# Kernel optimization log

Measured on AMD Instinct MI355X. Metric: run time of the kernel, lower is better.

The kernel has to match this reference:

```python
import jax, jax.numpy as jnp
import numpy as np
import math

N_CELLS = 16384
INPUT_DIM = 512
HIDDEN = 512


def build_neighbors(n):
    n_bits = max(1, int(math.ceil(math.log2(n))))
    idx = np.arange(n)
    flips = [idx ^ (1 << b) for b in range(n_bits)]
    ring = [(idx + 1) % n, (idx - 1) % n]
    allnb = np.stack(flips + ring, axis=1)
    # dedupe per row; for power-of-2 n every row has exactly n_bits+1 uniques
    rows = [sorted(set(r.tolist())) for r in allnb]
    return np.asarray(rows, dtype=np.int32)


def setup_inputs() -> dict:
    key = jax.random.key(0)
    ks = jax.random.split(key, 12)
    n, d, h = N_CELLS, INPUT_DIM, HIDDEN
    amp = jax.random.uniform(ks[0], (n, h)) * 0.5 + 0.5
    phase = jax.random.normal(ks[1], (n, h)) * 0.3 + (2 * math.pi * jnp.arange(n) / n)[:, None]
    return {
        "x": jax.random.normal(ks[2], (1, d), dtype=jnp.float32),
        "pump_W": jax.random.normal(ks[3], (n, d), dtype=jnp.float32) / np.sqrt(d),
        "pump_b": jax.random.normal(ks[4], (n,), dtype=jnp.float32) * 0.01,
        "dec_W": jax.random.normal(ks[5], (d, 2 * h), dtype=jnp.float32) / np.sqrt(2 * h),
        "dec_b": jax.random.normal(ks[6], (d,), dtype=jnp.float32) * 0.01,
        "cs_re": (amp * jnp.cos(phase)).astype(jnp.float32),
        "cs_im": (amp * jnp.sin(phase)).astype(jnp.float32),
        "excited": jax.random.uniform(ks[7], (n,)) * 0.6,  # some cells above 0.5 threshold
        "phase_vel": jax.random.normal(ks[8], (n, h), dtype=jnp.float32) * 0.05,
        "cav_re": jax.random.normal(ks[9], (h,), dtype=jnp.float32) * 0.01,
        "cav_im": jax.random.normal(ks[10], (h,), dtype=jnp.float32) * 0.01,
        "neighbors": jnp.asarray(build_neighbors(n)),
    }


def reference(x, pump_W, pump_b, dec_W, dec_b, cs_re, cs_im, excited, phase_vel, cav_re, cav_im, neighbors):
    states = (cs_re + 1j * cs_im).astype(jnp.complex64)          # [n,h]
    cavity = (cav_re + 1j * cav_im).astype(jnp.complex64)        # [h]

    # pump + excited fraction update
    pump = jax.nn.sigmoid(x @ pump_W.T + pump_b)[0]              # [n]
    excited = jnp.clip(excited * 0.95 + pump * 0.05, 0.0, 1.0)

    # free phase rotation: polar(1, 0.1*phase_vel)
    states = states * jnp.exp(1j * (phase_vel * 0.1)).astype(jnp.complex64)

    # neighbor phase coupling (hypercube + ring, k=15 neighbors each)
    ang = jnp.angle(states)                                      # [n,h]
    nb_states = states[neighbors]                                # [n,k,h]
    coupling = jnp.cos(ang[:, None, :] - ang[neighbors])         # [n,k,h]
    interference = 0.1 * jnp.sum(coupling * nb_states, axis=1)   # [n,h]
    k = neighbors.shape[1]
    new_states = 0.7 * states + 0.3 * interference / k

    # lasing: population inversion threshold
    lasing = excited > 0.5                                       # [n]
    n_lasing = jnp.sum(lasing)
    maskf = lasing.astype(jnp.float32)[:, None]
    # emission uses pre-phase-lock states (torch copies lasing_cells first)
    emission = jnp.sum(new_states * maskf, axis=0) / jnp.maximum(n_lasing, 1).astype(jnp.float32)
    cavity_new = jnp.where(n_lasing > 0, 0.8 * cavity + 0.2 * emission, cavity)

    # phase-lock lasing cells to (old) cavity phase
    cavity_phase = jnp.angle(cavity)                             # old cavity
    new_ang = jnp.angle(new_states)
    locked = 0.3 * cavity_phase[None, :] + 0.7 * new_ang
    locked_states = jnp.abs(new_states) * jnp.exp(1j * locked)
    new_states = jnp.where(lasing[:, None], locked_states.astype(jnp.complex64), new_states)
    excited = jnp.where(lasing, excited * 0.9, excited * 0.98)

    # cavity feedback (updated cavity) + amplitude renorm
    new_states = new_states + 0.05 * cavity_new[None, :]
    amp = jnp.abs(new_states)
    amp = amp / (jnp.max(amp, axis=-1, keepdims=True) + 1e-8)
    final_states = (amp * jnp.exp(1j * jnp.angle(new_states))).astype(jnp.complex64)

    # decode cavity mode
    out_real = jnp.concatenate([cavity_new.real, cavity_new.imag])[None, :].astype(jnp.float32)  # [1,2h]
    pred = out_real @ dec_W.T + dec_b                            # [1, input_dim]
    tension = jnp.var(jnp.abs(final_states))
    return pred, tension
```

## Files before the change

kernel.cpp:

```cpp
#include <hip/hip_runtime.h>
#include <hip/hip_fp16.h>
#include <math.h>

#define N_CELLS 16384
#define HID 512
#define IND 512

#define ROT_BLOCKS  2048
#define PUMP_BLOCKS 1024

#define CPB 16
#define CELL_BLOCKS (N_CELLS / CPB)
#define PRED_BLOCKS 128

#define CNT_OFF   0
#define LASB_OFF  1024
#define EMIS_OFF  8192
#define CAV_OFF   16384
#define VPART_OFF 32768
#define ROT_OFF   (1<<20)
#define NST_OFF   (ROT_OFF + (size_t)N_CELLS*HID*4)

typedef unsigned int u32;

__device__ inline __half2 u2h(u32 u) { union { u32 u; __half2 h; } x; x.u = u; return x.h; }
__device__ inline u32 h2u(__half2 h) { union { u32 u; __half2 h; } x; x.h = h; return x.u; }
__device__ inline u32 packh2(float re, float im) { return h2u(__floats2half2_rn(re, im)); }
__device__ inline float2 unph2(u32 u) { __half2 h = u2h(u); return make_float2(__low2float(h), __high2float(h)); }

#if __has_builtin(__builtin_amdgcn_fdot2)
typedef _Float16 hv2 __attribute__((ext_vector_type(2)));
__device__ inline float dot2u(u32 a, u32 b) {
    union { u32 u; hv2 h; } x, y; x.u = a; y.u = b;
    return __builtin_amdgcn_fdot2(x.h, y.h, 0.f, false);
}
#else
__device__ inline float dot2u(u32 a, u32 b) {
    float2 af = unph2(a), bf = unph2(b);
    return fmaf(af.x, bf.x, af.y * bf.y);
}
#endif

__device__ inline void accnb(__half2& acc, u32 y, u32 q) {
    float d = dot2u(y, q);
    acc = __hfma2(__float2half2_rn(d), u2h(q), acc);
}

__device__ inline u32 fincell(u32 y, __half2 acc, int las, float& emR, float& emI) {
    float2 yf = unph2(y);
    float a  = fmaf(yf.x, yf.x, yf.y * yf.y);
    float rs = rsqrtf(a);
    float sq = a * rs;
    float2 af = make_float2(__low2float(acc), __high2float(acc));
    float nr = 0.7f * sq * yf.x + 0.002f * rs * af.x;
    float ni = 0.7f * sq * yf.y + 0.002f * rs * af.y;
    if (las) { emR += nr; emI += ni; }
    return packh2(nr, ni);
}

__device__ inline u32 rot1(float re, float im, float w) {
    float sc = rsqrtf(sqrtf(fmaf(re, re, im * im)));
    float s, c;
    __sincosf(0.1f * w, &s, &c);
    return packh2((re * c - im * s) * sc, (re * s + im * c) * sc);
}

__device__ inline float dot4(float4 a, float4 b) {
    return a.x * b.x + a.y * b.y + a.z * b.z + a.w * b.w;
}

__global__ __launch_bounds__(256, 3) void k_front(const float* __restrict__ cr,
        const float* __restrict__ ci, const float* __restrict__ pv,
        u32* __restrict__ yt,
        const float* __restrict__ x, const float* __restrict__ pW,
        const float* __restrict__ pb, const float* __restrict__ excited,
        u32* __restrict__ lasb) {
    int b = blockIdx.x, tid = threadIdx.x;
    if (b < ROT_BLOCKS) {
        __shared__ u32 tile[64 * 65];
        int cb = b >> 3, hb = b & 7;
        const float4* cr4 = (const float4*)cr;
        const float4* ci4 = (const float4*)ci;
        const float4* pv4 = (const float4*)pv;
        float4 A[4], Bv[4], Wv[4];
        int row[4], c4[4];
#pragma unroll
        for (int j = 0; j < 4; ++j) {
            int idx = tid + 256 * j;
            row[j] = idx >> 4; c4[j] = idx & 15;
            size_t g = (size_t)(cb * 64 + row[j]) * 128 + hb * 16 + c4[j];
            A[j] = cr4[g]; Bv[j] = ci4[g]; Wv[j] = pv4[g];
        }
        __builtin_amdgcn_sched_barrier(0);
#pragma unroll
        for (int j = 0; j < 4; ++j) {
            u32* dst = &tile[row[j] * 65 + (c4[j] << 2)];
            dst[0] = rot1(A[j].x, Bv[j].x, Wv[j].x);
            dst[1] = rot1(A[j].y, Bv[j].y, Wv[j].y);
            dst[2] = rot1(A[j].z, Bv[j].z, Wv[j].z);
            dst[3] = rot1(A[j].w, Bv[j].w, Wv[j].w);
        }
        __syncthreads();
        uint4 v[4];
#pragma unroll
        for (int j = 0; j < 4; ++j) {
            int idx = tid + 256 * j;
            int chr = idx >> 4, q = idx & 15;
            v[j].x = tile[(q * 4 + 0) * 65 + chr];
            v[j].y = tile[(q * 4 + 1) * 65 + chr];
            v[j].z = tile[(q * 4 + 2) * 65 + chr];
            v[j].w = tile[(q * 4 + 3) * 65 + chr];
        }
#pragma unroll
        for (int j = 0; j < 4; ++j) {
            int idx = tid + 256 * j;
            int chr = idx >> 4, q = idx & 15;
            ((uint4*)(yt + (size_t)(hb * 64 + chr) * N_CELLS + cb * 64))[q] = v[j];
        }
    } else {
        int c0 = (b - ROT_BLOCKS) * 16;
        int cell = c0 + (tid >> 4);
        int l16 = tid & 15;
        int lane = tid & 63;
        const float4* w4 = (const float4*)(pW + (size_t)cell * IND);
        const float4* x4 = (const float4*)x;
        float4 wv[8];
#pragma unroll
        for (int k = 0; k < 8; ++k) wv[k] = w4[l16 + 16 * k];
        __builtin_amdgcn_sched_barrier(0);
        float acc = 0.f;
#pragma unroll
        for (int k = 0; k < 8; ++k) acc += dot4(wv[k], x4[l16 + 16 * k]);
#pragma unroll
        for (int o = 1; o < 16; o <<= 1) acc += __shfl_xor(acc, o, 64);
        int flag = 0;
        if (l16 == 0) {
            float p = 1.f / (1.f + expf(-(acc + pb[cell])));
            float e = excited[cell] * 0.95f + p * 0.05f;
            e = fminf(fmaxf(e, 0.f), 1.f);
            flag = (e > 0.5f) ? 1 : 0;
        }
        unsigned long long bal = __ballot(flag);
        if (lane == 0) {
            u32 val = (u32)(bal & 1) | ((u32)(bal >> 16) & 1) << 1
                    | ((u32)(bal >> 32) & 1) << 2 | ((u32)(bal >> 48) & 1) << 3;
            atomicOr(&lasb[cell >> 5], val << (cell & 31));
        }
    }
}

__global__ __launch_bounds__(1024, 8) void k_coup(const u32* __restrict__ yt,
                                                  const u32* __restrict__ lasb,
                                                  u32* __restrict__ nstT,
                                                  float2* __restrict__ emisT,
                                                  const float* __restrict__ cavr,
                                                  const float* __restrict__ cavi,
                                                  float* __restrict__ cavws,
                                                  int* __restrict__ cnt) {
    __shared__ __align__(16) u32 col[N_CELLS];
    int ch = blockIdx.x, tid = threadIdx.x;
    const uint4* src = (const uint4*)(yt + (size_t)ch * N_CELLS);
    uint4* cdst = (uint4*)col;
    {
        uint4 st[4];
#pragma unroll
        for (int k = 0; k < 4; ++k) st[k] = src[tid + 1024 * k];
        __builtin_amdgcn_sched_barrier(0);
#pragma unroll
        for (int k = 0; k < 4; ++k) cdst[tid + 1024 * k] = st[k];
    }
    __syncthreads();

    float emR = 0.f, emI = 0.f;
    int nlo = 0;
    uint4* outp = (uint4*)(nstT + (size_t)ch * N_CELLS);
#pragma unroll 2
    for (int j = 0; j < 4; ++j) {
        int s = tid + 1024 * j;
        u32 f = (lasb[s >> 3] >> ((s & 7) * 4)) & 0xF;
        int c = s << 2;
        uint4 sq = *(const uint4*)&col[c];
        __half2 z = __floats2half2_rn(0.f, 0.f);
        __half2 a0 = z, a1 = z, a2 = z, a3 = z;
#pragma unroll
        for (int bb = 2; bb < 14; ++bb) {
            uint4 q = *(const uint4*)&col[c ^ (1 << bb)];
            accnb(a0, sq.x, q.x);
            accnb(a1, sq.y, q.y);
            accnb(a2, sq.z, q.z);
            accnb(a3, sq.w, q.w);
        }
        u32 qm = col[(c - 1) & (N_CELLS - 1)];
        u32 qp = col[(c + 4) & (N_CELLS - 1)];
        accnb(a0, sq.x, sq.y); accnb(a0, sq.x, sq.z); accnb(a0, sq.x, qm);
        accnb(a1, sq.y, sq.x); accnb(a1, sq.y, sq.w); accnb(a1, sq.y, sq.z);
        accnb(a2, sq.z, sq.w); accnb(a2, sq.z, sq.x); accnb(a2, sq.z, sq.y);
        accnb(a3, sq.w, sq.z); accnb(a3, sq.w, sq.y); accnb(a3, sq.w, qp);
        nlo += __popc(f);
        uint4 ov;
        ov.x = fincell(sq.x, a0, f & 1, emR, emI);
        ov.y = fincell(sq.y, a1, f & 2, emR, emI);
        ov.z = fincell(sq.z, a2, f & 4, emR, emI);
        ov.w = fincell(sq.w, a3, f & 8, emR, emI);
        outp[s] = ov;
    }
    __syncthreads();
#pragma unroll
    for (int o = 32; o; o >>= 1) {
        emR += __shfl_xor(emR, o, 64);
        emI += __shfl_xor(emI, o, 64);
        nlo += __shfl_xor(nlo, o, 64);
    }
    float* scr = (float*)col;
    int* iscr = (int*)col;
    int wid = tid >> 6, lane = tid & 63;
    if (lane == 0) { scr[wid] = emR; scr[16 + wid] = emI; iscr[32 + wid] = nlo; }
    __syncthreads();
    if (tid == 0) {
        float sr = 0.f, si = 0.f; int sn = 0;
#pragma unroll
        for (int k = 0; k < 16; ++k) { sr += scr[k]; si += scr[16 + k]; sn += iscr[32 + k]; }
        emisT[ch] = make_float2(sr, si);
        iscr[48] = sn;
        __threadfence();
        int old = atomicAdd(cnt, 1);
        iscr[49] = (old == HID - 1) ? 1 : 0;
    }
    __syncthreads();
    if (iscr[49]) {
        __threadfence();
        int nl = iscr[48];
        float inv = (nl > 0) ? 0.2f / (float)nl : 0.f;
        if (tid < 512) {
            int i = tid;
            float crv = cavr[i], civ = cavi[i];
            float2 e = emisT[i];
            cavws[i]        = (nl > 0) ? 0.8f * crv + e.x * inv : crv;
            cavws[512 + i]  = (nl > 0) ? 0.8f * civ + e.y * inv : civ;
            cavws[1024 + i] = atan2f(civ, crv);
        }
    }
}

__global__ __launch_bounds__(256, 2) void k_finall(const u32* __restrict__ nstT,
        const u32* __restrict__ lasb, const float* __restrict__ cavws,
        const float* __restrict__ dW, const float* __restrict__ db,
        float2* __restrict__ vpart, int* __restrict__ cnt2,
        float* __restrict__ out) {
    int b = blockIdx.x, t = threadIdx.x;
    int wid = t >> 6, lane = t & 63;
    if (b < CELL_BLOCKS) {
        __shared__ __align__(16) u32 tile[CPB * HID];
        __shared__ __align__(16) float scav[1536];
        __shared__ float w1[4], w2[4];
        __shared__ int slast;
        __shared__ double l1s[4], l2s[4];

        int c0 = b * CPB;
        uint4 ld[8]; int chv[8], qv[8];
#pragma unroll
        for (int j = 0; j < 8; ++j) {
            int idx = t + 256 * j;
            chv[j] = idx >> 2; qv[j] = idx & 3;
            ld[j] = ((const uint4*)(nstT + (size_t)chv[j] * N_CELLS + c0))[qv[j]];
        }
        const float4* c4p = (const float4*)cavws;
#pragma unroll
        for (int k2 = 0; k2 < 2; ++k2) {
            int i = t + 256 * k2;
            if (i < 384) ((float4*)scav)[i] = c4p[i];
        }
        __builtin_amdgcn_sched_barrier(0);
#pragma unroll
        for (int j = 0; j < 8; ++j) {
#pragma unroll
            for (int e = 0; e < 4; ++e) {
                int cell = qv[j] * 4 + e;
                int sw = chv[j] ^ (((e ^ qv[j]) & 1) << 4);
                tile[cell * HID + sw] = ((const u32*)&ld[j])[e];
            }
        }
        __syncthreads();

        int cell = t >> 4, kk = t & 15;
        int cg = c0 + cell;
        int lasc = (lasb[cg >> 5] >> (cg & 31)) & 1;
        int swb = ((cell ^ (cell >> 2)) & 1) << 4;
        const u32* trow = &tile[cell * HID];
        float sa = 0.f, sa2 = 0.f, mx = 0.f;
#pragma unroll 8
        for (int i = 0; i < 32; ++i) {
            int ch = kk + 16 * i;
            float2 vf = unph2(trow[ch ^ swb]);
            float vx = vf.x, vy = vf.y;
            if (lasc) {
                float r = sqrtf(fmaf(vx, vx, vy * vy));
                float lk = 0.3f * scav[1024 + ch] + 0.7f * atan2f(vy, vx);
                float sn, cs;
                __sincosf(lk, &sn, &cs);
                vx = r * cs; vy = r * sn;
            }
            vx += 0.05f * scav[ch];
            vy += 0.05f * scav[512 + ch];
            float a2v = fmaf(vx, vx, vy * vy);
            float a = sqrtf(a2v);
            sa += a; sa2 += a2v; mx = fmaxf(mx, a);
        }
#pragma unroll
        for (int o = 1; o < 16; o <<= 1) {
            sa += __shfl_xor(sa, o, 64);
            sa2 += __shfl_xor(sa2, o, 64);
            mx = fmaxf(mx, __shfl_xor(mx, o, 64));
        }
        float invm = 1.f / (mx + 1e-8f);
        float s1 = sa * invm, s2 = sa2 * invm * invm;
        s1 += __shfl_xor(s1, 16, 64); s2 += __shfl_xor(s2, 16, 64);
        s1 += __shfl_xor(s1, 32, 64); s2 += __shfl_xor(s2, 32, 64);
        if (lane == 0) { w1[wid] = s1; w2[wid] = s2; }
        __syncthreads();
        if (t == 0) {
            vpart[b] = make_float2(w1[0] + w1[1] + w1[2] + w1[3],
                                   w2[0] + w2[1] + w2[2] + w2[3]);
            __threadfence();
            int old = atomicAdd(cnt2, 1);
            slast = (old == CELL_BLOCKS - 1) ? 1 : 0;
        }
        __syncthreads();
        if (slast) {
            __threadfence();
            double d1 = (double)vpart[t].x + (double)vpart[t + 256].x
                      + (double)vpart[t + 512].x + (double)vpart[t + 768].x;
            double d2 = (double)vpart[t].y + (double)vpart[t + 256].y
                      + (double)vpart[t + 512].y + (double)vpart[t + 768].y;
#pragma unroll
            for (int o = 32; o; o >>= 1) { d1 += __shfl_xor(d1, o, 64); d2 += __shfl_xor(d2, o, 64); }
            if (lane == 0) { l1s[wid] = d1; l2s[wid] = d2; }
            __syncthreads();
            if (t == 0) {
                double t1 = l1s[0] + l1s[1] + l1s[2] + l1s[3];
                double t2 = l2s[0] + l2s[1] + l2s[2] + l2s[3];
                double nn = (double)N_CELLS * (double)HID;
                double mean = t1 / nn;
                out[IND] = (float)(t2 / nn - mean * mean);
            }
        }
    } else {
        int j = (b - CELL_BLOCKS) * 4 + wid;
        const float4* w4 = (const float4*)(dW + (size_t)j * (2 * HID));
        const float4* o4 = (const float4*)cavws;
        float a2 = 0.f;
#pragma unroll
        for (int tt = 0; tt < 4; ++tt) {
            float4 a = w4[lane + 64 * tt];
            float4 bx = o4[lane + 64 * tt];
            a2 += a.x * bx.x + a.y * bx.y + a.z * bx.z + a.w * bx.w;
        }
#pragma unroll
        for (int o = 32; o; o >>= 1) a2 += __shfl_xor(a2, o, 64);
        if (lane == 0) out[j] = a2 + db[j];
    }
}

extern "C" void kernel_launch(void* const* d_in, const int* in_sizes, int n_in,
                              void* d_out, int out_size, void* d_ws, size_t ws_size,
                              hipStream_t stream) {
    const float* x       = (const float*)d_in[0];
    const float* pump_W  = (const float*)d_in[1];
    const float* pump_b  = (const float*)d_in[2];
    const float* dec_W   = (const float*)d_in[3];
    const float* dec_b   = (const float*)d_in[4];
    const float* cs_re   = (const float*)d_in[5];
    const float* cs_im   = (const float*)d_in[6];
    const float* excited = (const float*)d_in[7];
    const float* pvel    = (const float*)d_in[8];
    const float* cav_re  = (const float*)d_in[9];
    const float* cav_im  = (const float*)d_in[10];

    float* out = (float*)d_out;
    char* ws = (char*)d_ws;
    int*    cnt   = (int*)(ws + CNT_OFF);
    u32*    lasb  = (u32*)(ws + LASB_OFF);
    float2* emisT = (float2*)(ws + EMIS_OFF);
    float*  cavws = (float*)(ws + CAV_OFF);
    float2* vpart = (float2*)(ws + VPART_OFF);
    u32*    yt    = (u32*)(ws + ROT_OFF);
    u32*    nstT  = (u32*)(ws + NST_OFF);

    hipMemsetAsync(ws, 0, 4096, stream);
    k_front<<<ROT_BLOCKS + PUMP_BLOCKS, 256, 0, stream>>>(
        cs_re, cs_im, pvel, yt, x, pump_W, pump_b, excited, lasb);
    k_coup<<<HID, 1024, 0, stream>>>(yt, lasb, nstT, emisT, cav_re, cav_im, cavws, cnt);
    k_finall<<<CELL_BLOCKS + PRED_BLOCKS, 256, 0, stream>>>(
        nstT, lasb, cavws, dec_W, dec_b, vpart, cnt + 1, out);
}
```

Before: 264.5 us.

## Stage global loads directly into LDS and retile rotation and final kernels

Replaces register-staged global-to-shared copies with direct global_load_lds transfers in the rotation, coupling and finalize kernels. The rotation stage is retiled into smaller 64x32 tiles with twice as many blocks. The finalize kernel now uses a channel-major tile layout, so the per-cell max and sum reductions go through shared memory. Launch bounds are raised for higher occupancy. The aim is to cut VGPR pressure and LDS transpose overhead, at the cost of more LDS use and reliance on the LDS-direct load builtin.

```diff
diff --git a/kernel.cpp b/kernel.cpp
--- a/kernel.cpp
+++ b/kernel.cpp
@@ -6,7 +6,7 @@
 #define HID 512
 #define IND 512
 
-#define ROT_BLOCKS  2048
+#define ROT_BLOCKS  4096
 #define PUMP_BLOCKS 1024
 
 #define CPB 16
@@ -40,6 +40,17 @@
     return fmaf(af.x, bf.x, af.y * bf.y);
 }
 #endif
+
+__device__ inline void cp16(const void* g, void* l) {
+#if __has_builtin(__builtin_amdgcn_global_load_lds)
+    char* base = (char*)l - (size_t)((threadIdx.x & 63) * 16);
+    __builtin_amdgcn_global_load_lds(
+        (const __attribute__((address_space(1))) unsigned int*)g,
+        (__attribute__((address_space(3))) unsigned int*)base, 16, 0, 0);
+#else
+    *(uint4*)l = *(const uint4*)g;
+#endif
+}
 
 __device__ inline void accnb(__half2& acc, u32 y, u32 q) {
     float d = dot2u(y, q);
@@ -69,7 +80,7 @@
     return a.x * b.x + a.y * b.y + a.z * b.z + a.w * b.w;
 }
 
-__global__ __launch_bounds__(256, 3) void k_front(const float* __restrict__ cr,
+__global__ __launch_bounds__(256, 4) void k_front(const float* __restrict__ cr,
         const float* __restrict__ ci, const float* __restrict__ pv,
         u32* __restrict__ yt,
         const float* __restrict__ x, const float* __restrict__ pW,
@@ -77,45 +88,50 @@
         u32* __restrict__ lasb) {
     int b = blockIdx.x, tid = threadIdx.x;
     if (b < ROT_BLOCKS) {
-        __shared__ u32 tile[64 * 65];
-        int cb = b >> 3, hb = b & 7;
-        const float4* cr4 = (const float4*)cr;
-        const float4* ci4 = (const float4*)ci;
-        const float4* pv4 = (const float4*)pv;
-        float4 A[4], Bv[4], Wv[4];
-        int row[4], c4[4];
-#pragma unroll
-        for (int j = 0; j < 4; ++j) {
-            int idx = tid + 256 * j;
-            row[j] = idx >> 4; c4[j] = idx & 15;
-            size_t g = (size_t)(cb * 64 + row[j]) * 128 + hb * 16 + c4[j];
-            A[j] = cr4[g]; Bv[j] = ci4[g]; Wv[j] = pv4[g];
-        }
-        __builtin_amdgcn_sched_barrier(0);
-#pragma unroll
-        for (int j = 0; j < 4; ++j) {
-            u32* dst = &tile[row[j] * 65 + (c4[j] << 2)];
-            dst[0] = rot1(A[j].x, Bv[j].x, Wv[j].x);
-            dst[1] = rot1(A[j].y, Bv[j].y, Wv[j].y);
-            dst[2] = rot1(A[j].z, Bv[j].z, Wv[j].z);
-            dst[3] = rot1(A[j].w, Bv[j].w, Wv[j].w);
-        }
-        __syncthreads();
-        uint4 v[4];
-#pragma unroll
-        for (int j = 0; j < 4; ++j) {
-            int idx = tid + 256 * j;
-            int chr = idx >> 4, q = idx & 15;
-            v[j].x = tile[(q * 4 + 0) * 65 + chr];
-            v[j].y = tile[(q * 4 + 1) * 65 + chr];
-            v[j].z = tile[(q * 4 + 2) * 65 + chr];
-            v[j].w = tile[(q * 4 + 3) * 65 + chr];
-        }
-#pragma unroll
-        for (int j = 0; j < 4; ++j) {
-            int idx = tid + 256 * j;
-            int chr = idx >> 4, q = idx & 15;
-            ((uint4*)(yt + (size_t)(hb * 64 + chr) * N_CELLS + cb * 64))[q] = v[j];
+        __shared__ __align__(16) float sA[2048], sB[2048], sW[2048];
+        __shared__ __align__(16) u32 tile[32 * 65];
+        int cb = b >> 4, hb = b & 15;
+        size_t goff = (size_t)cb * 64 * 2048 + (size_t)hb * 128;
+        const char* gA = (const char*)cr + goff;
+        const char* gB = (const char*)ci + goff;
+        const char* gW = (const char*)pv + goff;
+#pragma unroll
+        for (int k = 0; k < 2; ++k) {
+            int o = tid * 16 + k * 4096;
+            size_t go = (size_t)(o >> 7) * 2048 + (o & 127);
+            cp16(gA + go, (char*)sA + o);
+            cp16(gB + go, (char*)sB + o);
+            cp16(gW + go, (char*)sW + o);
+        }
+        __syncthreads();
+        int cell = tid >> 2, q = tid & 3;
+        const float4* a4 = (const float4*)sA + cell * 8 + q * 2;
+        const float4* b4 = (const float4*)sB + cell * 8 + q * 2;
+        const float4* w4 = (const float4*)sW + cell * 8 + q * 2;
+        float4 A0 = a4[0], A1 = a4[1];
+        float4 B0 = b4[0], B1 = b4[1];
+        float4 W0 = w4[0], W1 = w4[1];
+        int ch8 = q * 8;
+        u32* tp = &tile[cell];
+        tp[(ch8 + 0) * 65] = rot1(A0.x, B0.x, W0.x);
+        tp[(ch8 + 1) * 65] = rot1(A0.y, B0.y, W0.y);
+        tp[(ch8 + 2) * 65] = rot1(A0.z, B0.z, W0.z);
+        tp[(ch8 + 3) * 65] = rot1(A0.w, B0.w, W0.w);
+        tp[(ch8 + 4) * 65] = rot1(A1.x, B1.x, W1.x);
+        tp[(ch8 + 5) * 65] = rot1(A1.y, B1.y, W1.y);
+        tp[(ch8 + 6) * 65] = rot1(A1.z, B1.z, W1.z);
+        tp[(ch8 + 7) * 65] = rot1(A1.w, B1.w, W1.w);
+        __syncthreads();
+#pragma unroll
+        for (int g2 = 0; g2 < 2; ++g2) {
+            int idx = tid + 256 * g2;
+            int chr = idx >> 4, c4 = idx & 15;
+            uint4 v;
+            v.x = tile[chr * 65 + c4 * 4 + 0];
+            v.y = tile[chr * 65 + c4 * 4 + 1];
+            v.z = tile[chr * 65 + c4 * 4 + 2];
+            v.w = tile[chr * 65 + c4 * 4 + 3];
+            ((uint4*)(yt + (size_t)(hb * 32 + chr) * N_CELLS + cb * 64))[c4] = v;
         }
     } else {
         int c0 = (b - ROT_BLOCKS) * 16;
@@ -127,7 +143,6 @@
         float4 wv[8];
 #pragma unroll
         for (int k = 0; k < 8; ++k) wv[k] = w4[l16 + 16 * k];
-        __builtin_amdgcn_sched_barrier(0);
         float acc = 0.f;
 #pragma unroll
         for (int k = 0; k < 8; ++k) acc += dot4(wv[k], x4[l16 + 16 * k]);
@@ -159,16 +174,10 @@
                                                   int* __restrict__ cnt) {
     __shared__ __align__(16) u32 col[N_CELLS];
     int ch = blockIdx.x, tid = threadIdx.x;
-    const uint4* src = (const uint4*)(yt + (size_t)ch * N_CELLS);
-    uint4* cdst = (uint4*)col;
-    {
-        uint4 st[4];
-#pragma unroll
-        for (int k = 0; k < 4; ++k) st[k] = src[tid + 1024 * k];
-        __builtin_amdgcn_sched_barrier(0);
-#pragma unroll
-        for (int k = 0; k < 4; ++k) cdst[tid + 1024 * k] = st[k];
-    }
+    const char* gsrc = (const char*)(yt + (size_t)ch * N_CELLS);
+#pragma unroll
+    for (int k = 0; k < 4; ++k)
+        cp16(gsrc + tid * 16 + k * 16384, (char*)col + tid * 16 + k * 16384);
     __syncthreads();
 
     float emR = 0.f, emI = 0.f;
@@ -242,27 +251,27 @@
     }
 }
 
-__global__ __launch_bounds__(256, 2) void k_finall(const u32* __restrict__ nstT,
+__global__ __launch_bounds__(256, 4) void k_finall(const u32* __restrict__ nstT,
         const u32* __restrict__ lasb, const float* __restrict__ cavws,
         const float* __restrict__ dW, const float* __restrict__ db,
         float2* __restrict__ vpart, int* __restrict__ cnt2,
         float* __restrict__ out) {
     int b = blockIdx.x, t = threadIdx.x;
-    int wid = t >> 6, lane = t & 63;
+    int w = t >> 6, lane = t & 63;
     if (b < CELL_BLOCKS) {
-        __shared__ __align__(16) u32 tile[CPB * HID];
+        __shared__ __align__(16) u32 tile2[HID * CPB];
         __shared__ __align__(16) float scav[1536];
-        __shared__ float w1[4], w2[4];
+        __shared__ float wm[4][16], ws1[4][16], ws2[4][16];
         __shared__ int slast;
         __shared__ double l1s[4], l2s[4];
 
         int c0 = b * CPB;
-        uint4 ld[8]; int chv[8], qv[8];
-#pragma unroll
-        for (int j = 0; j < 8; ++j) {
-            int idx = t + 256 * j;
-            chv[j] = idx >> 2; qv[j] = idx & 3;
-            ld[j] = ((const uint4*)(nstT + (size_t)chv[j] * N_CELLS + c0))[qv[j]];
+        const char* gbase = (const char*)nstT + (size_t)c0 * 4;
+#pragma unroll
+        for (int k = 0; k < 8; ++k) {
+            int o = t * 16 + k * 4096;
+            cp16(gbase + (size_t)(o >> 6) * (N_CELLS * 4) + (o & 63),
+                 (char*)tile2 + o);
         }
         const float4* c4p = (const float4*)cavws;
 #pragma unroll
@@ -270,28 +279,16 @@
             int i = t + 256 * k2;
             if (i < 384) ((float4*)scav)[i] = c4p[i];
         }
-        __builtin_amdgcn_sched_barrier(0);
-#pragma unroll
-        for (int j = 0; j < 8; ++j) {
-#pragma unroll
-            for (int e = 0; e < 4; ++e) {
-                int cell = qv[j] * 4 + e;
-                int sw = chv[j] ^ (((e ^ qv[j]) & 1) << 4);
-                tile[cell * HID + sw] = ((const u32*)&ld[j])[e];
-            }
-        }
-        __syncthreads();
-
-        int cell = t >> 4, kk = t & 15;
+        __syncthreads();
+
+        int cell = t & 15, chs = t >> 4;
         int cg = c0 + cell;
         int lasc = (lasb[cg >> 5] >> (cg & 31)) & 1;
-        int swb = ((cell ^ (cell >> 2)) & 1) << 4;
-        const u32* trow = &tile[cell * HID];
         float sa = 0.f, sa2 = 0.f, mx = 0.f;
 #pragma unroll 8
         for (int i = 0; i < 32; ++i) {
-            int ch = kk + 16 * i;
-            float2 vf = unph2(trow[ch ^ swb]);
+            int ch = chs + 16 * i;
+            float2 vf = unph2(tile2[ch * 16 + cell]);
             float vx = vf.x, vy = vf.y;
             if (lasc) {
                 float r = sqrtf(fmaf(vx, vx, vy * vy));
@@ -306,21 +303,27 @@
             float a = sqrtf(a2v);
             sa += a; sa2 += a2v; mx = fmaxf(mx, a);
         }
-#pragma unroll
-        for (int o = 1; o < 16; o <<= 1) {
-            sa += __shfl_xor(sa, o, 64);
-            sa2 += __shfl_xor(sa2, o, 64);
-            mx = fmaxf(mx, __shfl_xor(mx, o, 64));
-        }
-        float invm = 1.f / (mx + 1e-8f);
-        float s1 = sa * invm, s2 = sa2 * invm * invm;
-        s1 += __shfl_xor(s1, 16, 64); s2 += __shfl_xor(s2, 16, 64);
-        s1 += __shfl_xor(s1, 32, 64); s2 += __shfl_xor(s2, 32, 64);
-        if (lane == 0) { w1[wid] = s1; w2[wid] = s2; }
+        sa += __shfl_xor(sa, 16, 64); sa2 += __shfl_xor(sa2, 16, 64);
+        mx = fmaxf(mx, __shfl_xor(mx, 16, 64));
+        sa += __shfl_xor(sa, 32, 64); sa2 += __shfl_xor(sa2, 32, 64);
+        mx = fmaxf(mx, __shfl_xor(mx, 32, 64));
+        if (lane < 16) { wm[w][lane] = mx; ws1[w][lane] = sa; ws2[w][lane] = sa2; }
+        __syncthreads();
+        if (t < 16) {
+            float m = fmaxf(fmaxf(wm[0][t], wm[1][t]), fmaxf(wm[2][t], wm[3][t]));
+            float sA_ = ws1[0][t] + ws1[1][t] + ws1[2][t] + ws1[3][t];
+            float sB_ = ws2[0][t] + ws2[1][t] + ws2[2][t] + ws2[3][t];
+            float invm = 1.f / (m + 1e-8f);
+            float s1 = sA_ * invm, s2 = sB_ * invm * invm;
+#pragma unroll
+            for (int o = 1; o < 16; o <<= 1) {
+                s1 += __shfl_xor(s1, o, 64);
+                s2 += __shfl_xor(s2, o, 64);
+            }
+            if (t == 0) vpart[b] = make_float2(s1, s2);
+        }
         __syncthreads();
         if (t == 0) {
-            vpart[b] = make_float2(w1[0] + w1[1] + w1[2] + w1[3],
-                                   w2[0] + w2[1] + w2[2] + w2[3]);
             __threadfence();
             int old = atomicAdd(cnt2, 1);
             slast = (old == CELL_BLOCKS - 1) ? 1 : 0;
@@ -334,7 +337,7 @@
                       + (double)vpart[t + 512].y + (double)vpart[t + 768].y;
 #pragma unroll
             for (int o = 32; o; o >>= 1) { d1 += __shfl_xor(d1, o, 64); d2 += __shfl_xor(d2, o, 64); }
-            if (lane == 0) { l1s[wid] = d1; l2s[wid] = d2; }
+            if (lane == 0) { l1s[w] = d1; l2s[w] = d2; }
             __syncthreads();
             if (t == 0) {
                 double t1 = l1s[0] + l1s[1] + l1s[2] + l1s[3];
@@ -345,7 +348,7 @@
             }
         }
     } else {
-        int j = (b - CELL_BLOCKS) * 4 + wid;
+        int j = (b - CELL_BLOCKS) * 4 + w;
         const float4* w4 = (const float4*)(dW + (size_t)j * (2 * HID));
         const float4* o4 = (const float4*)cavws;
         float a2 = 0.f;
```

Result: no change. 262.9 us (-0.6%).
